# Performance work log

Measured on AMD Instinct MI355X. Metric: run time of the kernel, lower is better.

The kernel has to match this reference:

```python
import jax, jax.numpy as jnp
import numpy as np

N = 50000       # nodes
E = 800000      # edges (avg degree 16)
HID = 128       # hidden_size
H = 8           # num_heads
DH = HID // H   # head_dim = 16


def setup_inputs() -> dict:
    key = jax.random.key(0)
    ks = jax.random.split(key, 9)
    wscale = (1.0 / HID) ** 0.5  # ~ torch Linear init scale
    inp = {
        "h": jax.random.normal(ks[0], (N, HID), jnp.float32),
        "val": jnp.ones((E,), jnp.float32),          # A.val (adjacency values)
        "Wq": jax.random.normal(ks[1], (HID, HID), jnp.float32) * wscale,
        "bq": jax.random.normal(ks[2], (HID,), jnp.float32) * wscale,
        "Wk": jax.random.normal(ks[3], (HID, HID), jnp.float32) * wscale,
        "bk": jax.random.normal(ks[4], (HID,), jnp.float32) * wscale,
        "Wv": jax.random.normal(ks[5], (HID, HID), jnp.float32) * wscale,
        "bv": jax.random.normal(ks[6], (HID,), jnp.float32) * wscale,
        "src": jax.random.randint(ks[7], (E,), 0, N, jnp.int32),
        "dst": jax.random.randint(ks[8], (E,), 0, N, jnp.int32),
    }
    return inp


def reference(h, val, Wq, bq, Wk, bk, Wv, bv, src, dst):
    scaling = DH ** (-0.5)
    # projections (torch Linear: x @ W.T + b), reshape (N, head_dim, num_heads)
    q = (h @ Wq.T + bq).reshape(N, DH, H) * scaling
    k = (h @ Wk.T + bk).reshape(N, DH, H)
    v = (h @ Wv.T + bv).reshape(N, DH, H)
    # bsddmm: per-edge per-head scores, masked/scaled by adjacency values
    score = jnp.einsum("edh,edh->eh", q[src], k[dst]) * val[:, None]  # [E, H]
    # sparse per-row softmax (stable, segment-wise over src rows)
    m = jax.ops.segment_max(score, src, num_segments=N)               # [N, H]
    p = jnp.exp(score - m[src])
    s = jax.ops.segment_sum(p, src, num_segments=N)                   # [N, H]
    attn = p / s[src]                                                 # [E, H]
    # bspmm: weighted aggregation of v over edges
    out = jax.ops.segment_sum(attn[:, None, :] * v[dst], src, num_segments=N)  # [N, DH, H]
    return out.reshape(N, HID)
```

## Files before the change

### kernel.cpp

```cpp
#include <hip/hip_runtime.h>
#include <hip/hip_bf16.h>
#include <math.h>

#define HID 128
#define NH  8
#define SCHUNK 512
#define TPAD 136

typedef __attribute__((ext_vector_type(8))) short short8;
typedef __attribute__((ext_vector_type(4))) float f32x4;

static __device__ __forceinline__ float blo(unsigned int u) {
  union { unsigned int i; float f; } c; c.i = u << 16; return c.f;
}
static __device__ __forceinline__ float bhi(unsigned int u) {
  union { unsigned int i; float f; } c; c.i = u & 0xFFFF0000u; return c.f;
}
static __device__ __forceinline__ unsigned short f2bf(float f) {
  union { float f; unsigned int i; } c; c.f = f;
  unsigned int r = c.i + 0x7FFFu + ((c.i >> 16) & 1u);
  return (unsigned short)(r >> 16);
}

static __device__ __forceinline__ short8 ldconv8(const float* __restrict__ p) {
  float4 x = *(const float4*)p;
  float4 y = *(const float4*)(p + 4);
  short8 r;
  r[0] = (short)f2bf(x.x); r[1] = (short)f2bf(x.y);
  r[2] = (short)f2bf(x.z); r[3] = (short)f2bf(x.w);
  r[4] = (short)f2bf(y.x); r[5] = (short)f2bf(y.y);
  r[6] = (short)f2bf(y.z); r[7] = (short)f2bf(y.w);
  return r;
}

__global__ void convert3_kernel(const float* __restrict__ s0, const float* __restrict__ s1,
                                const float* __restrict__ s2,
                                unsigned short* __restrict__ dst, int n8,
                                int* __restrict__ deg, int n) {
  if (blockIdx.y == 3) {
    for (int i = blockIdx.x * blockDim.x + threadIdx.x; i < n;
         i += gridDim.x * blockDim.x)
      deg[i] = 0;
    return;
  }
  const float* s = (blockIdx.y == 0) ? s0 : (blockIdx.y == 1) ? s1 : s2;
  unsigned short* d = dst + (size_t)blockIdx.y * n8 * 8;
  for (int i = blockIdx.x * blockDim.x + threadIdx.x; i < n8;
       i += gridDim.x * blockDim.x) {
    float4 a = ((const float4*)s)[2 * i];
    float4 b = ((const float4*)s)[2 * i + 1];
    uint4 o;
    o.x = ((unsigned int)f2bf(a.y) << 16) | f2bf(a.x);
    o.y = ((unsigned int)f2bf(a.w) << 16) | f2bf(a.z);
    o.z = ((unsigned int)f2bf(b.y) << 16) | f2bf(b.x);
    o.w = ((unsigned int)f2bf(b.w) << 16) | f2bf(b.z);
    ((uint4*)d)[i] = o;
  }
}

__global__ __launch_bounds__(256) void proj_hist(
    const float* __restrict__ h, const unsigned short* __restrict__ wb,
    const float* __restrict__ bq, const float* __restrict__ bk,
    const float* __restrict__ bv,
    unsigned short* __restrict__ qb, unsigned short* __restrict__ kvb,
    const int* __restrict__ src, int* __restrict__ deg, int* __restrict__ rank,
    int n, int bp, int e) {
  __shared__ unsigned short tile[4][16][TPAD];

  if (blockIdx.x >= (unsigned)(3 * bp)) {
    int i = (blockIdx.x - 3 * bp) * 256 + threadIdx.x;
    if (i < e) rank[i] = atomicAdd(&deg[src[i]], 1);
    return;
  }

  const int y = blockIdx.x / bp;
  const int bxx = blockIdx.x - y * bp;
  const unsigned short* W = wb + (size_t)y * HID * HID;
  const float* bias = (y == 0) ? bq : (y == 1) ? bk : bv;
  const float scale = (y == 0) ? 0.25f : 1.0f;

  unsigned short* out;
  int ostride;
  if (y == 0)      { out = qb;        ostride = HID; }
  else if (y == 1) { out = kvb;       ostride = 2 * HID; }
  else             { out = kvb + HID; ostride = 2 * HID; }

  const int lane = threadIdx.x & 63;
  const int wave = threadIdx.x >> 6;
  const int n0 = bxx * 64 + wave * 16;

  int arow = n0 + (lane & 15);
  if (arow > n - 1) arow = n - 1;
  const int koff = (lane >> 4) * 8;

  const float* hr = h + (size_t)arow * HID + koff;
  short8 a0 = ldconv8(hr +  0);
  short8 a1 = ldconv8(hr + 32);
  short8 a2 = ldconv8(hr + 64);
  short8 a3 = ldconv8(hr + 96);

#pragma unroll
  for (int ct = 0; ct < 8; ++ct) {
    const int c = ct * 16 + (lane & 15);
    const unsigned short* wr = W + (size_t)c * HID + koff;
    f32x4 acc = {0.f, 0.f, 0.f, 0.f};
    acc = __builtin_amdgcn_mfma_f32_16x16x32_bf16(a0, *(const short8*)(wr +  0), acc, 0, 0, 0);
    acc = __builtin_amdgcn_mfma_f32_16x16x32_bf16(a1, *(const short8*)(wr + 32), acc, 0, 0, 0);
    acc = __builtin_amdgcn_mfma_f32_16x16x32_bf16(a2, *(const short8*)(wr + 64), acc, 0, 0, 0);
    acc = __builtin_amdgcn_mfma_f32_16x16x32_bf16(a3, *(const short8*)(wr + 96), acc, 0, 0, 0);

    const float bb = bias[c];
    const int cp = (c & 7) * 16 + (c >> 3);
#pragma unroll
    for (int r = 0; r < 4; ++r) {
      int rl = (lane >> 4) * 4 + r;
      tile[wave][rl][cp] = f2bf((acc[r] + bb) * scale);
    }
  }

#pragma unroll
  for (int p = 0; p < 4; ++p) {
    int rl = p * 4 + (lane >> 4);
    int row = n0 + rl;
    if (row < n) {
      uint4 vv = *(const uint4*)&tile[wave][rl][(lane & 15) * 8];
      *(uint4*)(out + (size_t)row * ostride + (lane & 15) * 8) = vv;
    }
  }
}

__global__ __launch_bounds__(256) void reduce_blocks(
    const int* __restrict__ deg, int* __restrict__ partials, int n) {
  __shared__ int sm[256];
  int base = blockIdx.x * SCHUNK;
  int t = threadIdx.x;
  int i0 = base + t, i1 = base + t + 256;
  int s = ((i0 < n) ? deg[i0] : 0) + ((i1 < n) ? deg[i1] : 0);
  sm[t] = s;
  __syncthreads();
  for (int off = 128; off > 0; off >>= 1) {
    if (t < off) sm[t] += sm[t + off];
    __syncthreads();
  }
  if (t == 0) partials[blockIdx.x] = sm[0];
}

__global__ __launch_bounds__(256) void scan_all(
    const int* __restrict__ deg, const int* __restrict__ partials,
    int* __restrict__ rowptr, int nb, int n) {
  __shared__ int ps[256];
  __shared__ int wsum[4];
  int t = threadIdx.x;
  int pv = (t < nb) ? partials[t] : 0;
  ps[t] = pv;
  __syncthreads();
  for (int off = 1; off < 256; off <<= 1) {
    int u = (t >= off) ? ps[t - off] : 0;
    __syncthreads();
    ps[t] += u;
    __syncthreads();
  }
  const int b = blockIdx.x;
  int myoff = ps[b] - partials[b];
  int total = ps[nb - 1];

  int base = b * SCHUNK;
  int lane = t & 63, wave = t >> 6;
  int i0 = base + 2 * t, i1 = i0 + 1;
  int d0 = (i0 < n) ? deg[i0] : 0;
  int d1 = (i1 < n) ? deg[i1] : 0;
  int s = d0 + d1;
  int incl = s;
#pragma unroll
  for (int off = 1; off < 64; off <<= 1) {
    int u = __shfl_up(incl, off);
    if (lane >= off) incl += u;
  }
  if (lane == 63) wsum[wave] = incl;
  __syncthreads();
  int woff = 0;
  for (int w = 0; w < wave; ++w) woff += wsum[w];
  int excl = woff + (incl - s) + myoff;
  if (i0 < n) rowptr[i0] = excl;
  if (i1 < n) rowptr[i1] = excl + d0;
  if (b == nb - 1 && t == 0) rowptr[n] = total;
}

__global__ void scatter_kernel(const int* __restrict__ src, const int* __restrict__ dst,
                               const float* __restrict__ val, const int* __restrict__ rank,
                               const int* __restrict__ rowptr,
                               unsigned int* __restrict__ csr, int e) {
  int i = blockIdx.x * blockDim.x + threadIdx.x;
  int e2 = e >> 1;
  if (i < e2) {
    int2 s2 = ((const int2*)src)[i];
    int2 d2 = ((const int2*)dst)[i];
    float2 v2 = ((const float2*)val)[i];
    int2 r2 = ((const int2*)rank)[i];
    unsigned int p0 = ((unsigned int)d2.x & 0xFFFFu) | ((unsigned int)f2bf(v2.x) << 16);
    unsigned int p1 = ((unsigned int)d2.y & 0xFFFFu) | ((unsigned int)f2bf(v2.y) << 16);
    csr[rowptr[s2.x] + r2.x] = p0;
    csr[rowptr[s2.y] + r2.y] = p1;
  } else if (i == e2 && (e & 1)) {
    int j = e - 1;
    csr[rowptr[src[j]] + rank[j]] =
        ((unsigned int)dst[j] & 0xFFFFu) | ((unsigned int)f2bf(val[j]) << 16);
  }
}

__global__ __launch_bounds__(256) void node_kernel(
    const unsigned short* __restrict__ qb, const unsigned short* __restrict__ kvb,
    const int* __restrict__ rowptr, const unsigned int* __restrict__ csr,
    float* __restrict__ out, int n) {
  int wid = (blockIdx.x * blockDim.x + threadIdx.x) >> 6;
  int lane = threadIdx.x & 63;
  if (wid >= n) return;
  const int head = lane & 7;
  const int eg = lane >> 3;

  const uint4* qr = (const uint4*)(qb + (size_t)wid * HID + head * 16);
  uint4 q0 = qr[0], q1 = qr[1];
  float qf[16];
  {
    unsigned int qd[8] = {q0.x, q0.y, q0.z, q0.w, q1.x, q1.y, q1.z, q1.w};
#pragma unroll
    for (int j = 0; j < 8; ++j) { qf[2 * j] = blo(qd[j]); qf[2 * j + 1] = bhi(qd[j]); }
  }

  int beg = rowptr[wid], end = rowptr[wid + 1];
  float m = -INFINITY, s = 0.f;
  float o[16];
#pragma unroll
  for (int j = 0; j < 16; ++j) o[j] = 0.f;

  for (int base = beg; base < end; base += 8) {
    int i = base + eg;
    bool valid = i < end;
    unsigned int rec = valid ? csr[i] : 0u;
    int d = rec & 0xFFFFu;
    if (d > n - 1) d = n - 1;
    float vale = bhi(rec);

    const uint4* kr = (const uint4*)(kvb + (size_t)d * (2 * HID) + head * 16);
    uint4 ka = kr[0], kb2 = kr[1];
    uint4 va = kr[16], vb2 = kr[17];

    float dot = 0.f;
    {
      unsigned int kd[8] = {ka.x, ka.y, ka.z, ka.w, kb2.x, kb2.y, kb2.z, kb2.w};
#pragma unroll
      for (int j = 0; j < 8; ++j)
        dot += qf[2 * j] * blo(kd[j]) + qf[2 * j + 1] * bhi(kd[j]);
    }
    float score = valid ? dot * vale : -INFINITY;

    float mx = score;
    mx = fmaxf(mx, __shfl_xor(mx, 8));
    mx = fmaxf(mx, __shfl_xor(mx, 16));
    mx = fmaxf(mx, __shfl_xor(mx, 32));

    if (!__all(mx <= m + 8.f)) {
      float mn = fmaxf(m, mx);
      float c = __expf(m - mn);
      s *= c;
#pragma unroll
      for (int j = 0; j < 16; ++j) o[j] *= c;
      m = mn;
    }

    float w = __expf(score - m);
    s += w;
    {
      unsigned int vd[8] = {va.x, va.y, va.z, va.w, vb2.x, vb2.y, vb2.z, vb2.w};
#pragma unroll
      for (int j = 0; j < 8; ++j) {
        o[2 * j]     += w * blo(vd[j]);
        o[2 * j + 1] += w * bhi(vd[j]);
      }
    }
  }

  s += __shfl_xor(s, 8); s += __shfl_xor(s, 16); s += __shfl_xor(s, 32);
#pragma unroll
  for (int j = 0; j < 16; ++j) {
    o[j] += __shfl_xor(o[j], 8);
    o[j] += __shfl_xor(o[j], 16);
    o[j] += __shfl_xor(o[j], 32);
  }

  float inv = (s > 0.f) ? 1.f / s : 0.f;
#pragma unroll
  for (int dd = 0; dd < 16; ++dd) {
    if (eg == (dd & 7))
      out[(size_t)wid * HID + dd * 8 + head] = o[dd] * inv;
  }
}

static inline size_t align16(size_t x) { return (x + 15) & ~(size_t)15; }

extern "C" void kernel_launch(void* const* d_in, const int* in_sizes, int n_in,
                              void* d_out, int out_size, void* d_ws, size_t ws_size,
                              hipStream_t stream) {
  const float* h  = (const float*)d_in[0];
  const float* val = (const float*)d_in[1];
  const float* Wq = (const float*)d_in[2];
  const float* bq = (const float*)d_in[3];
  const float* Wk = (const float*)d_in[4];
  const float* bk = (const float*)d_in[5];
  const float* Wv = (const float*)d_in[6];
  const float* bv = (const float*)d_in[7];
  const int* src  = (const int*)d_in[8];
  const int* dst  = (const int*)d_in[9];

  int N = in_sizes[0] / HID;
  int E = in_sizes[8];
  float* out = (float*)d_out;
  int nb = (N + SCHUNK - 1) / SCHUNK;

  size_t base = (size_t)d_ws;
  size_t off = 0;
  unsigned short* wb  = (unsigned short*)(base + off);  off = align16(off + (size_t)3 * HID * HID * 2);
  unsigned short* qb  = (unsigned short*)(base + off);  off = align16(off + (size_t)N * HID * 2);
  unsigned short* kvb = (unsigned short*)(base + off);  off = align16(off + (size_t)2 * N * HID * 2);
  int* rowptr  = (int*)(base + off);                    off = align16(off + (size_t)(N + 1) * 4);
  int* deg     = (int*)(base + off);                    off = align16(off + (size_t)N * 4);
  int* partials = (int*)(base + off);                   off = align16(off + (size_t)nb * 4);
  int* rank    = (int*)(base + off);                    off = align16(off + (size_t)E * 4);
  unsigned int* csr = (unsigned int*)(base + off);      off = align16(off + (size_t)E * 4);

  int n8_w = HID * HID / 8;
  convert3_kernel<<<dim3((n8_w + 255) / 256, 4), 256, 0, stream>>>(
      Wq, Wk, Wv, wb, n8_w, deg, N);

  int bp = (N + 63) / 64;
  int he = (E + 255) / 256;
  proj_hist<<<3 * bp + he, 256, 0, stream>>>(
      h, wb, bq, bk, bv, qb, kvb, src, deg, rank, N, bp, E);

  reduce_blocks<<<nb, 256, 0, stream>>>(deg, partials, N);
  scan_all<<<nb, 256, 0, stream>>>(deg, partials, rowptr, nb, N);
  scatter_kernel<<<((E / 2) + 256) / 256, 256, 0, stream>>>(
      src, dst, val, rank, rowptr, csr, E);

  node_kernel<<<(N + 3) / 4, 256, 0, stream>>>(qb, kvb, rowptr, csr, out, N);
}
```

Before: 162.2 us.

## Replicate degree histogram across eight copies to reduce atomic contention

The per-row degree counting atomics are spread over eight replicated histograms, chosen by edge block index. A combine kernel then turns the replicas into per-replica exclusive offsets plus a total degree. The scatter step adds the replica offset to each edge's rank. The aim is to cut same-address atomic contention, at the cost of extra zeroing, an extra read/write pass over 8N ints, and an additional gather in scatter.

```diff
diff --git a/kernel.cpp b/kernel.cpp
--- a/kernel.cpp
+++ b/kernel.cpp
@@ -4,6 +4,7 @@
 
 #define HID 128
 #define NH  8
+#define NR  8
 #define SCHUNK 512
 #define TPAD 136
 
@@ -36,11 +37,11 @@
 __global__ void convert3_kernel(const float* __restrict__ s0, const float* __restrict__ s1,
                                 const float* __restrict__ s2,
                                 unsigned short* __restrict__ dst, int n8,
-                                int* __restrict__ deg, int n) {
+                                int* __restrict__ degR, int nzero) {
   if (blockIdx.y == 3) {
-    for (int i = blockIdx.x * blockDim.x + threadIdx.x; i < n;
+    for (int i = blockIdx.x * blockDim.x + threadIdx.x; i < nzero;
          i += gridDim.x * blockDim.x)
-      deg[i] = 0;
+      degR[i] = 0;
     return;
   }
   const float* s = (blockIdx.y == 0) ? s0 : (blockIdx.y == 1) ? s1 : s2;
@@ -63,13 +64,17 @@
     const float* __restrict__ bq, const float* __restrict__ bk,
     const float* __restrict__ bv,
     unsigned short* __restrict__ qb, unsigned short* __restrict__ kvb,
-    const int* __restrict__ src, int* __restrict__ deg, int* __restrict__ rank,
+    const int* __restrict__ src, int* __restrict__ degR, int* __restrict__ rank,
     int n, int bp, int e) {
   __shared__ unsigned short tile[4][16][TPAD];
 
   if (blockIdx.x >= (unsigned)(3 * bp)) {
-    int i = (blockIdx.x - 3 * bp) * 256 + threadIdx.x;
-    if (i < e) rank[i] = atomicAdd(&deg[src[i]], 1);
+    int b = blockIdx.x - 3 * bp;
+    int i = b * 256 + threadIdx.x;
+    if (i < e) {
+      int* dr = degR + (size_t)(b & (NR - 1)) * n;
+      rank[i] = atomicAdd(&dr[src[i]], 1);
+    }
     return;
   }
 
@@ -129,14 +134,37 @@
   }
 }
 
-__global__ __launch_bounds__(256) void reduce_blocks(
-    const int* __restrict__ deg, int* __restrict__ partials, int n) {
+__global__ __launch_bounds__(256) void reduce_combine(
+    int* __restrict__ degR, int* __restrict__ deg,
+    int* __restrict__ partials, int n) {
   __shared__ int sm[256];
   int base = blockIdx.x * SCHUNK;
   int t = threadIdx.x;
   int i0 = base + t, i1 = base + t + 256;
-  int s = ((i0 < n) ? deg[i0] : 0) + ((i1 < n) ? deg[i1] : 0);
-  sm[t] = s;
+  int s0 = 0, s1 = 0;
+  if (i0 < n) {
+    int acc = 0;
+#pragma unroll
+    for (int r = 0; r < NR; ++r) {
+      size_t idx = (size_t)r * n + i0;
+      int v = degR[idx];
+      degR[idx] = acc;
+      acc += v;
+    }
+    deg[i0] = acc; s0 = acc;
+  }
+  if (i1 < n) {
+    int acc = 0;
+#pragma unroll
+    for (int r = 0; r < NR; ++r) {
+      size_t idx = (size_t)r * n + i1;
+      int v = degR[idx];
+      degR[idx] = acc;
+      acc += v;
+    }
+    deg[i1] = acc; s1 = acc;
+  }
+  sm[t] = s0 + s1;
   __syncthreads();
   for (int off = 128; off > 0; off >>= 1) {
     if (t < off) sm[t] += sm[t + off];
@@ -188,8 +216,8 @@
 
 __global__ void scatter_kernel(const int* __restrict__ src, const int* __restrict__ dst,
                                const float* __restrict__ val, const int* __restrict__ rank,
-                               const int* __restrict__ rowptr,
-                               unsigned int* __restrict__ csr, int e) {
+                               const int* __restrict__ rowptr, const int* __restrict__ degR,
+                               unsigned int* __restrict__ csr, int e, int n) {
   int i = blockIdx.x * blockDim.x + threadIdx.x;
   int e2 = e >> 1;
   if (i < e2) {
@@ -197,13 +225,17 @@
     int2 d2 = ((const int2*)dst)[i];
     float2 v2 = ((const float2*)val)[i];
     int2 r2 = ((const int2*)rank)[i];
+    int rr = ((2 * i) >> 8) & (NR - 1);
+    const int* dr = degR + (size_t)rr * n;
     unsigned int p0 = ((unsigned int)d2.x & 0xFFFFu) | ((unsigned int)f2bf(v2.x) << 16);
     unsigned int p1 = ((unsigned int)d2.y & 0xFFFFu) | ((unsigned int)f2bf(v2.y) << 16);
-    csr[rowptr[s2.x] + r2.x] = p0;
-    csr[rowptr[s2.y] + r2.y] = p1;
+    csr[rowptr[s2.x] + dr[s2.x] + r2.x] = p0;
+    csr[rowptr[s2.y] + dr[s2.y] + r2.y] = p1;
   } else if (i == e2 && (e & 1)) {
     int j = e - 1;
-    csr[rowptr[src[j]] + rank[j]] =
+    int rr = (j >> 8) & (NR - 1);
+    int s = src[j];
+    csr[rowptr[s] + degR[(size_t)rr * n + s] + rank[j]] =
         ((unsigned int)dst[j] & 0xFFFFu) | ((unsigned int)f2bf(val[j]) << 16);
   }
 }
@@ -324,23 +356,24 @@
   unsigned short* kvb = (unsigned short*)(base + off);  off = align16(off + (size_t)2 * N * HID * 2);
   int* rowptr  = (int*)(base + off);                    off = align16(off + (size_t)(N + 1) * 4);
   int* deg     = (int*)(base + off);                    off = align16(off + (size_t)N * 4);
+  int* degR    = (int*)(base + off);                    off = align16(off + (size_t)NR * N * 4);
   int* partials = (int*)(base + off);                   off = align16(off + (size_t)nb * 4);
   int* rank    = (int*)(base + off);                    off = align16(off + (size_t)E * 4);
   unsigned int* csr = (unsigned int*)(base + off);      off = align16(off + (size_t)E * 4);
 
   int n8_w = HID * HID / 8;
-  convert3_kernel<<<dim3((n8_w + 255) / 256, 4), 256, 0, stream>>>(
-      Wq, Wk, Wv, wb, n8_w, deg, N);
+  convert3_kernel<<<dim3(128, 4), 256, 0, stream>>>(
+      Wq, Wk, Wv, wb, n8_w, degR, NR * N);
 
   int bp = (N + 63) / 64;
   int he = (E + 255) / 256;
   proj_hist<<<3 * bp + he, 256, 0, stream>>>(
-      h, wb, bq, bk, bv, qb, kvb, src, deg, rank, N, bp, E);
-
-  reduce_blocks<<<nb, 256, 0, stream>>>(deg, partials, N);
+      h, wb, bq, bk, bv, qb, kvb, src, degR, rank, N, bp, E);
+
+  reduce_combine<<<nb, 256, 0, stream>>>(degR, deg, partials, N);
   scan_all<<<nb, 256, 0, stream>>>(deg, partials, rowptr, nb, N);
   scatter_kernel<<<((E / 2) + 256) / 256, 256, 0, stream>>>(
-      src, dst, val, rank, rowptr, csr, E);
+      src, dst, val, rank, rowptr, degR, csr, E, N);
 
   node_kernel<<<(N + 3) / 4, 256, 0, stream>>>(qb, kvb, rowptr, csr, out, N);
 }
```

Result: no change. 165.5 us (+2.0%).
